# Optimization experiments

Measured on AMD Instinct MI355X. Metric: run time of the kernel, lower is better.

## Reference

```python
import jax, jax.numpy as jnp
import numpy as np
import math

IN_DIM = 128
NUM_BEV = 128
HEIGHT, WIDTH, DEPTH = 200, 176, 2  # pos_table dims: grid_size[1]//8, grid_size[0]//8, 2
PLANES = IN_DIM  # SA_block planes


def make_pos_table():
    d_model = IN_DIM
    pe = np.zeros((d_model, HEIGHT, WIDTH, DEPTH), dtype=np.float32)
    dm = int(math.ceil(d_model / 3))
    if dm % 2:
        dm += 1
    div_term = np.exp(np.arange(0.0, dm, 2) * -(math.log(10000.0) / dm))
    div_term_depth = np.exp(np.arange(0.0, dm - 2, 2) * -(math.log(10000.0) / dm - 2))
    pos_w = np.arange(0.0, WIDTH)[:, None]
    pos_h = np.arange(0.0, HEIGHT)[:, None]
    pos_d = np.arange(0.0, DEPTH)[:, None]
    sw = np.sin(pos_w * div_term).T  # [dm/2, W]
    cw = np.cos(pos_w * div_term).T
    sh = np.sin(pos_h * div_term).T  # [dm/2, H]
    ch = np.cos(pos_h * div_term).T
    sd = np.sin(pos_d * div_term_depth).T  # [.., D]
    cd = np.cos(pos_d * div_term_depth).T
    pe[0:dm:2] = np.broadcast_to(sw[:, None, :, None], (sw.shape[0], HEIGHT, WIDTH, DEPTH))
    pe[1:dm:2] = np.broadcast_to(cw[:, None, :, None], (cw.shape[0], HEIGHT, WIDTH, DEPTH))
    pe[dm:2 * dm:2] = np.broadcast_to(sh[:, :, None, None], (sh.shape[0], HEIGHT, WIDTH, DEPTH))
    pe[dm + 1:2 * dm:2] = np.broadcast_to(ch[:, :, None, None], (ch.shape[0], HEIGHT, WIDTH, DEPTH))
    n_rem_s = pe[2 * dm::2].shape[0]
    n_rem_c = pe[2 * dm + 1::2].shape[0]
    pe[2 * dm::2] = np.broadcast_to(sd[:n_rem_s, None, None, :], (n_rem_s, HEIGHT, WIDTH, DEPTH))
    pe[2 * dm + 1::2] = np.broadcast_to(cd[:n_rem_c, None, None, :], (n_rem_c, HEIGHT, WIDTH, DEPTH))
    return jnp.asarray(pe)


def sa_block(x, params):
    # x: [C, N] single-batch non-local self-attention (SA-Det3D SA_block)
    # q,k: C -> C/2 via 1x1 "conv" (matmul), grouped softmax attention, v: C -> C/2, out: C/2 -> C, residual
    r = PLANES // 2
    q = params['wq'] @ x   # [r, N]
    k = params['wk'] @ x   # [r, N]
    v = params['wv'] @ x   # [r, N]
    # scaled dot-product attention over N (groups=1 simplification of kernel_channel attention)
    q = q / jnp.sqrt(jnp.asarray(r, x.dtype))
    att = jax.nn.softmax(q.T @ k, axis=-1)  # [N, N]
    out = v @ att.T                           # [r, N]
    out = params['wo'] @ out                  # [C, N]
    # BN in eval with default init ~ identity (gamma=1, beta=0, running stats 0/1)
    return out + x


def layer_norm(x, gamma, beta, eps=1e-6):
    mu = jnp.mean(x, axis=-1, keepdims=True)
    var = jnp.var(x, axis=-1, keepdims=True)
    return (x - mu) * jax.lax.rsqrt(var + eps) * gamma + beta


def setup_inputs() -> dict:
    key = jax.random.key(0)
    ks = jax.random.split(key, 12)
    N, B = 32768, 4
    nper = N // B
    voxel_feats = jax.random.normal(ks[0], (N, IN_DIM), dtype=jnp.float32)
    b = jnp.repeat(jnp.arange(B, dtype=jnp.int32), nper)
    cz = jax.random.randint(ks[1], (N,), 0, 2, dtype=jnp.int32)
    cy = jax.random.randint(ks[2], (N,), 0, HEIGHT, dtype=jnp.int32)
    cx = jax.random.randint(ks[3], (N,), 0, WIDTH, dtype=jnp.int32)
    coords = jnp.stack([b, cz, cy, cx], axis=1)
    r = PLANES // 2
    sd = 1.0 / np.sqrt(IN_DIM)
    def mk(k, shape, s):
        return jax.random.normal(k, shape, dtype=jnp.float32) * s
    p1 = {'wq': mk(ks[4], (r, IN_DIM), sd), 'wk': mk(ks[5], (r, IN_DIM), sd),
          'wv': mk(ks[6], (r, IN_DIM), sd), 'wo': mk(ks[7], (IN_DIM, r), 1.0 / np.sqrt(r))}
    p2 = {'wq': mk(ks[8], (r, IN_DIM), sd), 'wk': mk(ks[9], (r, IN_DIM), sd),
          'wv': mk(ks[10], (r, IN_DIM), sd), 'wo': mk(ks[11], (IN_DIM, r), 1.0 / np.sqrt(r))}
    return {
        'voxel_feats': voxel_feats,
        'coords': coords,
        'ln_gamma': jnp.ones((IN_DIM,), jnp.float32),
        'ln_beta': jnp.zeros((IN_DIM,), jnp.float32),
        'attn1_wq': p1['wq'], 'attn1_wk': p1['wk'], 'attn1_wv': p1['wv'], 'attn1_wo': p1['wo'],
        'attn2_wq': p2['wq'], 'attn2_wk': p2['wk'], 'attn2_wv': p2['wv'], 'attn2_wo': p2['wo'],
        'nx': 176, 'ny': 200, 'nz': 2, 'batch_size': 4,
    }


def bilinear_down2(x):
    # F.interpolate(scale_factor=0.5, mode='bilinear', align_corners=False)
    B, C, H, W = x.shape
    return x.reshape(B, C, H // 2, 2, W // 2, 2).mean(axis=(3, 5))


def reference(voxel_feats, coords, ln_gamma, ln_beta,
              attn1_wq, attn1_wk, attn1_wv, attn1_wo,
              attn2_wq, attn2_wk, attn2_wv, attn2_wo,
              nx, ny, nz, batch_size):
    pos_table = make_pos_table()
    # positional encoding gather: pos_table[:, y, x, z] -> [C, N] -> [N, C]
    pe = pos_table[:, coords[:, 2], coords[:, 3], coords[:, 1]].T
    x = voxel_feats + jax.lax.stop_gradient(pe)
    x = layer_norm(x, ln_gamma, ln_beta)  # dropout in eval = identity

    N = x.shape[0]
    nper = N // batch_size  # fixed voxels per batch (setup guarantees contiguous equal split)
    p1 = {'wq': attn1_wq, 'wk': attn1_wk, 'wv': attn1_wv, 'wo': attn1_wo}
    p2 = {'wq': attn2_wq, 'wk': attn2_wk, 'wv': attn2_wv, 'wo': attn2_wo}

    xb = x.reshape(batch_size, nper, IN_DIM).transpose(0, 2, 1)  # [B, C, n]
    def per_batch(xc):
        return sa_block(sa_block(xc, p1), p2)
    yb = jax.vmap(per_batch)(xb)  # [B, C, n]

    cb = coords.reshape(batch_size, nper, 4)
    indices = (cb[:, :, 1] + cb[:, :, 2] * nx + cb[:, :, 3]).astype(jnp.int32)  # [B, n]
    grid = nz * nx * ny
    spatial = jnp.zeros((batch_size, NUM_BEV, grid), dtype=x.dtype)
    spatial = spatial.at[jnp.arange(batch_size)[:, None], :, indices].set(
        yb.transpose(0, 2, 1))
    out = spatial.reshape(batch_size, NUM_BEV * nz, ny, nx)
    out_half = bilinear_down2(out)
    return out, out_half
```

## Files before the change

kernel.cpp:

```cpp
#include <hip/hip_runtime.h>
#include <cmath>
#include <algorithm>

typedef __bf16 bf16x8 __attribute__((ext_vector_type(8)));
typedef float  f32x4  __attribute__((ext_vector_type(4)));
typedef unsigned int u32x2 __attribute__((ext_vector_type(2)));

struct TabArgs { double dt[22]; double dtd[21]; };

__device__ __forceinline__ unsigned short f2bf(float f) {
  unsigned int u = __float_as_uint(f);
  u += 0x7FFFu + ((u >> 16) & 1u);
  return (unsigned short)(u >> 16);
}

union U8 { uint4 u4; u32x2 d2[2]; unsigned short s[8]; bf16x8 b; };

__device__ __forceinline__ bf16x8 pack8(float4 a, float4 b) {
  U8 u;
  u.s[0] = f2bf(a.x); u.s[1] = f2bf(a.y); u.s[2] = f2bf(a.z); u.s[3] = f2bf(a.w);
  u.s[4] = f2bf(b.x); u.s[5] = f2bf(b.y); u.s[6] = f2bf(b.z); u.s[7] = f2bf(b.w);
  return u.b;
}

__device__ __forceinline__ f32x4 mfma16(bf16x8 a, bf16x8 b, f32x4 c) {
  return __builtin_amdgcn_mfma_f32_16x16x32_bf16(a, b, c, 0, 0, 0);
}

__device__ __forceinline__ unsigned ldso(const void* p) {
  return (unsigned)(unsigned long long)(const __attribute__((address_space(3))) void*)p;
}
__device__ __forceinline__ void gll16(const void* g, void* l) {
  __builtin_amdgcn_global_load_lds(
      (const __attribute__((address_space(1))) unsigned int*)g,
      (__attribute__((address_space(3))) unsigned int*)l, 16, 0, 0);
}
__device__ __forceinline__ u32x2 trd(unsigned addr) {
  u32x2 d;
  asm volatile("ds_read_b64_tr_b16 %0, %1" : "=v"(d) : "v"(addr) : "memory");
  return d;
}
__device__ __forceinline__ unsigned cvtpk(float lo, float hi) {
  unsigned r;
  asm("v_cvt_pk_bf16_f32 %0, %1, %2" : "=v"(r) : "v"(lo), "v"(hi));
  return r;
}

#define WSTRIDE 35264

__global__ __launch_bounds__(256) void k_tab(float* __restrict__ tab, TabArgs ta) {
  int t = blockIdx.x * 256 + threadIdx.x;
  if (t >= 16624) return;
  double arg; int odd;
  if (t < 7744) {
    int pos = t / 44, c = t - pos * 44; odd = c & 1;
    arg = (double)pos * ta.dt[c >> 1];
  } else if (t < 16544) {
    int u = t - 7744; int pos = u / 44, c = u - pos * 44; odd = c & 1;
    arg = (double)pos * ta.dt[c >> 1];
  } else {
    int u = t - 16544; int z = u / 40, c = u - z * 40; odd = c & 1;
    arg = z ? ta.dtd[c >> 1] : 0.0;
  }
  tab[t] = (float)(odd ? cos(arg) : sin(arg));
}

__global__ __launch_bounds__(256) void k_peln(const float* __restrict__ vox, const int* __restrict__ coords,
                                              const float* __restrict__ gamma, const float* __restrict__ beta,
                                              const float* __restrict__ tab, float* __restrict__ xo) {
  int wave = threadIdx.x >> 6, lane = threadIdx.x & 63;
  int n = blockIdx.x * 4 + wave;
  int cz = coords[n * 4 + 1], cy = coords[n * 4 + 2], cx = coords[n * 4 + 3];
  int c0 = lane, c1 = lane + 64;
  float p0 = (c0 < 44) ? tab[cx * 44 + c0] : tab[7744 + cy * 44 + (c0 - 44)];
  float p1 = (c1 < 88) ? tab[7744 + cy * 44 + (c1 - 44)] : tab[16544 + cz * 40 + (c1 - 88)];
  float x0 = vox[n * 128 + c0] + p0;
  float x1 = vox[n * 128 + c1] + p1;
  float s = x0 + x1, q = x0 * x0 + x1 * x1;
  #pragma unroll
  for (int o = 1; o < 64; o <<= 1) { s += __shfl_xor(s, o); q += __shfl_xor(q, o); }
  float mu  = s * 0.0078125f;
  float var = q * 0.0078125f - mu * mu;
  float inv = 1.0f / sqrtf(var + 1e-6f);
  xo[n * 128 + c0] = (x0 - mu) * inv * gamma[c0] + beta[c0];
  xo[n * 128 + c1] = (x1 - mu) * inv * gamma[c1] + beta[c1];
}

__global__ __launch_bounds__(192) void k_qkv(const float* __restrict__ X,
    const float* __restrict__ wq, const float* __restrict__ wk, const float* __restrict__ wv,
    unsigned short* __restrict__ Qo, unsigned short* __restrict__ Ko, unsigned short* __restrict__ Vo) {
  __shared__ uint4 xs4[1024];
  char* xs = (char*)xs4;
  int base = blockIdx.x * 64;
  for (int t = threadIdx.x; t < 1024; t += 192) {
    int row = t >> 4, ch = t & 15;
    const float* src = X + (base + row) * 128 + ch * 8;
    U8 u; u.b = pack8(*(const float4*)src, *(const float4*)(src + 4));
    *(uint4*)(xs + ((row * 256 + ch * 16) ^ ((row & 7) << 4))) = u.u4;
  }
  __syncthreads();
  int w = threadIdx.x >> 6, ln = threadIdx.x & 63, g = ln >> 4, l15 = ln & 15;
  const float* W = (w == 0) ? wq : (w == 1) ? wk : wv;
  unsigned short* O = (w == 0) ? Qo : (w == 1) ? Ko : Vo;
  f32x4 z = {0.f, 0.f, 0.f, 0.f};
  f32x4 acc[4][4];
  #pragma unroll
  for (int i = 0; i < 4; i++)
    #pragma unroll
    for (int j = 0; j < 4; j++) acc[i][j] = z;
  for (int ks = 0; ks < 4; ks++) {
    bf16x8 bf[4];
    #pragma unroll
    for (int nb = 0; nb < 4; nb++) {
      const float* wp = W + (nb * 16 + l15) * 128 + ks * 32 + g * 8;
      bf[nb] = pack8(*(const float4*)wp, *(const float4*)(wp + 4));
    }
    #pragma unroll
    for (int mb = 0; mb < 4; mb++) {
      bf16x8 af = *(const bf16x8*)(xs + (((mb * 16 + l15) * 256 + ks * 64 + g * 16) ^ ((l15 & 7) << 4)));
      #pragma unroll
      for (int nb = 0; nb < 4; nb++) acc[mb][nb] = mfma16(af, bf[nb], acc[mb][nb]);
    }
  }
  float sc = (w == 0) ? 0.125f : 1.0f;
  #pragma unroll
  for (int mb = 0; mb < 4; mb++)
    #pragma unroll
    for (int nb = 0; nb < 4; nb++)
      #pragma unroll
      for (int r = 0; r < 4; r++)
        O[(base + mb * 16 + g * 4 + r) * 64 + nb * 16 + l15] = f2bf(acc[mb][nb][r] * sc);
}

__global__ __launch_bounds__(256) void k_flash(const unsigned short* __restrict__ Qp,
    const unsigned short* __restrict__ Kp, const unsigned short* __restrict__ Vp,
    const float* __restrict__ wo, const float* __restrict__ Xin, float* __restrict__ Xout) {
  __shared__ __align__(16) char lds[40960];
  const int bid0 = blockIdx.x;
  const int bid = ((bid0 & 7) << 6) | (bid0 >> 3);
  const int qt = bid & 127, b = bid >> 7;
  const int tid = threadIdx.x;
  const int w = tid >> 6, g = (tid >> 4) & 3, l15 = tid & 15;
  const int wrow = b * 8192 + qt * 64 + w * 16;
  const int swz = (l15 & 7) << 4;
  const unsigned lb = ldso(lds);
  char* PbC = lds + 32768 + w * 2048;
  const unsigned PbA = lb + 32768u + (unsigned)w * 2048u;

  bf16x8 qf0 = *(const bf16x8*)(Qp + (wrow + l15) * 64 + g * 8);
  bf16x8 qf1 = *(const bf16x8*)(Qp + (wrow + l15) * 64 + 32 + g * 8);

  f32x4 zz = {0.f, 0.f, 0.f, 0.f};
  f32x4 o[4]; float mr[4], lr[4];
  #pragma unroll
  for (int i = 0; i < 4; i++) { o[i] = zz; mr[i] = -INFINITY; lr[i] = 0.f; }

  const int kvb0 = b * 8192;

#define STAGE(T) do {                                                          \
    int kvb_ = kvb0 + (T) * 64;                                                \
    unsigned db_ = (unsigned)((T) & 1) * 16384u;                               \
    _Pragma("unroll")                                                          \
    for (int t0 = 0; t0 < 2; t0++) {                                           \
      int u_ = tid + t0 * 256;                                                 \
      int row_ = u_ >> 3, c_ = u_ & 7;                                         \
      gll16(Kp + (kvb_ + row_) * 64 + ((c_ ^ (row_ & 7)) * 8),                 \
            lds + db_ + (unsigned)(w * 64 + t0 * 256) * 16u);                  \
      int row2_ = ((u_ >> 5) << 2) | ((u_ >> 1) & 3);                          \
      int ch2_ = (((u_ >> 3) & 3) << 1) | (u_ & 1);                            \
      gll16(Vp + (kvb_ + row2_) * 64 + ch2_ * 8,                               \
            lds + db_ + 8192u + (unsigned)(w * 64 + t0 * 256) * 16u);          \
    }                                                                          \
  } while (0)

  STAGE(0);
  __syncthreads();

  for (int kt = 0; kt < 128; kt++) {
    const unsigned kbB = (unsigned)(kt & 1) * 16384u;
    const unsigned vbB = kbB + 8192u;
    if (kt < 127) STAGE(kt + 1);

    f32x4 s[4];
    #pragma unroll
    for (int kb = 0; kb < 4; kb++) {
      bf16x8 kf0 = *(const bf16x8*)(lds + kbB + (unsigned)((((kb * 16 + l15) * 128 + g * 16) ^ swz)));
      bf16x8 kf1 = *(const bf16x8*)(lds + kbB + (unsigned)((((kb * 16 + l15) * 128 + 64 + g * 16) ^ swz)));
      s[kb] = mfma16(qf0, kf0, zz);
      s[kb] = mfma16(qf1, kf1, s[kb]);
    }
    float al[4];
    #pragma unroll
    for (int r = 0; r < 4; r++) {
      float mx = fmaxf(fmaxf(s[0][r], s[1][r]), fmaxf(s[2][r], s[3][r]));
      #pragma unroll
      for (int off = 1; off < 16; off <<= 1) mx = fmaxf(mx, __shfl_xor(mx, off));
      float mn = fmaxf(mr[r], mx);
      al[r] = __expf(mr[r] - mn);
      float p0 = __expf(s[0][r] - mn), p1 = __expf(s[1][r] - mn);
      float p2 = __expf(s[2][r] - mn), p3 = __expf(s[3][r] - mn);
      s[0][r] = p0; s[1][r] = p1; s[2][r] = p2; s[3][r] = p3;
      lr[r] = lr[r] * al[r] + ((p0 + p1) + (p2 + p3));
      mr[r] = mn;
    }
    #pragma unroll
    for (int db = 0; db < 4; db++)
      #pragma unroll
      for (int r = 0; r < 4; r++) o[db][r] *= al[r];

    #pragma unroll
    for (int kb = 0; kb < 4; kb++) {
      u32x2 pw;
      pw.x = cvtpk(s[kb][0], s[kb][1]);
      pw.y = cvtpk(s[kb][2], s[kb][3]);
      *(u32x2*)(PbC + (kb * 4 + (l15 >> 2)) * 128 + (l15 & 3) * 32 + g * 8) = pw;
    }
    asm volatile("s_waitcnt lgkmcnt(0)" ::: "memory");
    __builtin_amdgcn_sched_barrier(0);

    #pragma unroll
    for (int kc = 0; kc < 2; kc++) {
      unsigned preg = PbA + (unsigned)((kc * 8 + g * 2) * 128 + l15 * 8);
      u32x2 pa0 = trd(preg);
      u32x2 pa1 = trd(preg + 128u);
      unsigned vreg = lb + vbB + (unsigned)((kc * 8 + g * 2) * 512 + l15 * 8);
      u32x2 v00 = trd(vreg);          u32x2 v01 = trd(vreg + 512u);
      u32x2 v10 = trd(vreg + 128u);   u32x2 v11 = trd(vreg + 640u);
      u32x2 v20 = trd(vreg + 256u);   u32x2 v21 = trd(vreg + 768u);
      u32x2 v30 = trd(vreg + 384u);   u32x2 v31 = trd(vreg + 896u);
      asm volatile("s_waitcnt lgkmcnt(0)" ::: "memory");
      __builtin_amdgcn_sched_barrier(0);
      U8 ua;  ua.d2[0] = pa0;  ua.d2[1] = pa1;
      U8 u0;  u0.d2[0] = v00;  u0.d2[1] = v01;
      U8 u1;  u1.d2[0] = v10;  u1.d2[1] = v11;
      U8 u2;  u2.d2[0] = v20;  u2.d2[1] = v21;
      U8 u3;  u3.d2[0] = v30;  u3.d2[1] = v31;
      o[0] = mfma16(ua.b, u0.b, o[0]);
      o[1] = mfma16(ua.b, u1.b, o[1]);
      o[2] = mfma16(ua.b, u2.b, o[2]);
      o[3] = mfma16(ua.b, u3.b, o[3]);
    }
    __syncthreads();
  }

  #pragma unroll
  for (int r = 0; r < 4; r++)
    #pragma unroll
    for (int off = 1; off < 16; off <<= 1) lr[r] += __shfl_xor(lr[r], off);
  float iv[4];
  #pragma unroll
  for (int r = 0; r < 4; r++) iv[r] = 1.0f / lr[r];
  #pragma unroll
  for (int db = 0; db < 4; db++)
    #pragma unroll
    for (int r = 0; r < 4; r++) {
      int q = g * 4 + r;
      *(unsigned short*)(PbC + ((q * 128 + (db * 16 + l15) * 2) ^ ((q & 7) << 4))) = f2bf(o[db][r] * iv[r]);
    }
  __syncthreads();
  f32x4 a2[8];
  #pragma unroll
  for (int cb = 0; cb < 8; cb++) a2[cb] = zz;
  #pragma unroll
  for (int ksx = 0; ksx < 2; ksx++) {
    bf16x8 oa = *(const bf16x8*)(PbC + ((l15 * 128 + ksx * 64 + g * 16) ^ swz));
    #pragma unroll
    for (int cb = 0; cb < 8; cb++) {
      const float* wp = wo + (cb * 16 + l15) * 64 + ksx * 32 + g * 8;
      a2[cb] = mfma16(oa, pack8(*(const float4*)wp, *(const float4*)(wp + 4)), a2[cb]);
    }
  }
  #pragma unroll
  for (int cb = 0; cb < 8; cb++)
    #pragma unroll
    for (int r = 0; r < 4; r++) {
      int row = wrow + g * 4 + r, col = cb * 16 + l15;
      Xout[row * 128 + col] = a2[cb][r] + Xin[row * 128 + col];
    }
#undef STAGE
}

__global__ __launch_bounds__(256) void k_win(const int* __restrict__ coords, int* __restrict__ win) {
  int n = blockIdx.x * 256 + threadIdx.x;
  int b = n >> 13, j = n & 8191;
  int cz = coords[n * 4 + 1], cy = coords[n * 4 + 2], cx = coords[n * 4 + 3];
  int idx = cz + cy * 176 + cx;
  atomicMax(&win[b * WSTRIDE + idx], j);
}

__global__ __launch_bounds__(256) void k_gp(const int* __restrict__ win, const float* __restrict__ X,
                                            float* __restrict__ out, float* __restrict__ half_) {
  unsigned tid = blockIdx.x * 256u + threadIdx.x;
  unsigned b = tid / 2252800u;
  unsigned f = tid % 2252800u;
  unsigned ch2 = f / 8800u;
  unsigned rem = f % 8800u;
  unsigned yh = rem / 88u, xh = rem % 88u;
  unsigned c = ch2 >> 1;
  unsigned zoff = (ch2 & 1u) * 35200u;
  const int* wb = win + b * WSTRIDE;
  const float* Xb = X + (unsigned long long)b * 8192u * 128u + c;
  unsigned y0 = 2u * yh, x0 = 2u * xh;
  float v[4];
  #pragma unroll
  for (int dy = 0; dy < 2; dy++)
    #pragma unroll
    for (int dx = 0; dx < 2; dx++) {
      unsigned gcell = zoff + (y0 + dy) * 176u + (x0 + dx);
      float val = 0.f;
      if (gcell <= 35200u) {
        int j = wb[gcell];
        if (j >= 0) val = Xb[(unsigned)j * 128u];
      }
      v[dy * 2 + dx] = val;
    }
  float* ob = out + (((unsigned long long)(b * 256u + ch2)) * 200u + y0) * 176u + x0;
  ob[0] = v[0]; ob[1] = v[1]; ob[176] = v[2]; ob[177] = v[3];
  half_[tid] = 0.25f * ((v[0] + v[1]) + (v[2] + v[3]));
}

namespace ddm {
struct dd { double h, l; };
static inline dd qts(double a, double b) { double s = a + b; return {s, b - (s - a)}; }
static inline dd tsum(double a, double b) {
  double s = a + b, bb = s - a; return {s, (a - (s - bb)) + (b - bb)};
}
static inline dd tprod(double a, double b) { double p = a * b; return {p, std::fma(a, b, -p)}; }
static inline dd dadd(dd a, dd b) { dd s = tsum(a.h, b.h); double l = s.l + a.l + b.l; return qts(s.h, l); }
static inline dd dmul(dd a, dd b) {
  dd p = tprod(a.h, b.h); double l = p.l + (a.h * b.l + a.l * b.h); return qts(p.h, l);
}
static inline dd dmuld(dd a, double b) { dd p = tprod(a.h, b); double l = p.l + a.l * b; return qts(p.h, l); }
static inline dd dinv(double n) { double h = 1.0 / n; double l = std::fma(-h, n, 1.0) / n; return {h, l}; }
static inline dd dsqrt(dd a) {
  double s = std::sqrt(a.h);
  dd s2 = tprod(s, s);
  dd e = dadd(a, {-s2.h, -s2.l});
  double c = (e.h + e.l) / (2.0 * s);
  return qts(s, c);
}
struct ExpCtx {
  dd ln2_64;
  dd tab[64];
  ExpCtx() {
    dd third = dinv(3.0);
    dd t2 = dmul(third, third);
    dd pw = third, s = {0.0, 0.0};
    for (int k = 0; k < 42; k++) {
      s = dadd(s, dmul(pw, dinv((double)(2 * k + 1))));
      pw = dmul(pw, t2);
    }
    dd ln2 = {2.0 * s.h, 2.0 * s.l};
    ln2_64 = {ln2.h / 64.0, ln2.l / 64.0};
    dd r = {2.0, 0.0};
    for (int i = 0; i < 6; i++) r = dsqrt(r);
    tab[0] = {1.0, 0.0};
    for (int j = 1; j < 64; j++) tab[j] = dmul(tab[j - 1], r);
  }
  double exp(double x) const {
    if (x == 0.0) return 1.0;
    double m = std::nearbyint(x * (64.0 / 0.6931471805599453));
    dd r = dadd({x, 0.0}, dmuld(ln2_64, -m));
    dd s = {1.0, 0.0}, term = {1.0, 0.0};
    for (int k = 1; k <= 13; k++) {
      term = dmul(term, r);
      term = dmul(term, dinv((double)k));
      s = dadd(s, term);
    }
    long mi = (long)m;
    long e = mi >> 6;
    long j = mi & 63;
    dd v = dmul(tab[j], s);
    return std::scalbn(v.h + v.l, (int)e);
  }
};
}

extern "C" void kernel_launch(void* const* d_in, const int* in_sizes, int n_in,
                              void* d_out, int out_size, void* d_ws, size_t ws_size,
                              hipStream_t stream) {
  const float* vox   = (const float*)d_in[0];
  const int*   coords= (const int*)d_in[1];
  const float* gam   = (const float*)d_in[2];
  const float* bet   = (const float*)d_in[3];
  const float* w1q = (const float*)d_in[4], *w1k = (const float*)d_in[5];
  const float* w1v = (const float*)d_in[6], *w1o = (const float*)d_in[7];
  const float* w2q = (const float*)d_in[8], *w2k = (const float*)d_in[9];
  const float* w2v = (const float*)d_in[10], *w2o = (const float*)d_in[11];
  float* out = (float*)d_out;
  char* ws = (char*)d_ws;

  float* tab  = (float*)(ws);
  int*   win  = (int*)(ws + 69632);
  float* bufA = (float*)(ws + 1048576);
  float* bufB = (float*)(ws + 18874368);
  unsigned short* Q = (unsigned short*)(ws + 37748736);
  unsigned short* K = (unsigned short*)(ws + 41943040);
  unsigned short* V = (unsigned short*)(ws + 46137344);

  ddm::ExpCtx ec;
  TabArgs ta;
  double lg = std::log(10000.0);
  double t1 = -(lg / 44.0);
  double t2 = -(lg / 44.0 - 2.0);
  for (int i = 0; i < 22; i++) ta.dt[i]  = ec.exp((double)(2 * i) * t1);
  for (int i = 0; i < 21; i++) ta.dtd[i] = ec.exp((double)(2 * i) * t2);

  {
    const double E0 = 0.245;
    const int RANK = 0;
    struct Cand { double score; int i; int d; };
    Cand cands[20]; int nc = 0;
    for (int i = 10; i <= 19; i++) {
      double c = ta.dtd[i];
      double u = std::nextafter(c, 1e300) - c;
      for (int d = -1; d <= 1; d += 2) {
        double cp = c + (double)d * u;
        double es = std::fabs(std::sin(cp) - std::sin(c));
        double ecs = std::fabs(std::cos(cp) - std::cos(c));
        double e = es > ecs ? es : ecs;
        cands[nc++] = { std::fabs(e - E0), i, d };
      }
    }
    std::sort(cands, cands + nc, [](const Cand& a, const Cand& b){ return a.score < b.score; });
    if (RANK < nc) {
      double c = ta.dtd[cands[RANK].i];
      double u = std::nextafter(c, 1e300) - c;
      ta.dtd[cands[RANK].i] = c + (double)cands[RANK].d * u;
    }
  }

  hipMemsetAsync(win, 0xFF, 4 * WSTRIDE * sizeof(int), stream);
  hipLaunchKernelGGL(k_tab,   dim3(65),     dim3(256), 0, stream, tab, ta);
  hipLaunchKernelGGL(k_peln,  dim3(8192),   dim3(256), 0, stream, vox, coords, gam, bet, tab, bufA);
  hipLaunchKernelGGL(k_qkv,   dim3(512),    dim3(192), 0, stream, bufA, w1q, w1k, w1v, Q, K, V);
  hipLaunchKernelGGL(k_flash, dim3(512),    dim3(256), 0, stream, Q, K, V, w1o, bufA, bufB);
  hipLaunchKernelGGL(k_qkv,   dim3(512),    dim3(192), 0, stream, bufB, w2q, w2k, w2v, Q, K, V);
  hipLaunchKernelGGL(k_flash, dim3(512),    dim3(256), 0, stream, Q, K, V, w2o, bufB, bufA);
  hipLaunchKernelGGL(k_win,   dim3(128),    dim3(256), 0, stream, coords, win);
  hipLaunchKernelGGL(k_gp,    dim3(35200),  dim3(256), 0, stream, win, bufA, out, out + 36044800);
}
```

Measured before the change: 677.6 us.

## Widen flash KV tiles to 128, defer rescaling, use exp2 and DPP reductions

The flash-attention loop now stages 128 keys per iteration instead of 64, halving the number of iterations and barriers, with LDS doubled to 80KB. The Q scale folds in log2(e) so softmax can use the raw v_exp_f32 instruction. Row max and sum reductions use DPP row_ror instead of shuffles. The running max and output rescale are skipped unless some row's max grows by more than 8. P·V transposed LDS reads are double-buffered with partial waitcnts, and setprio is placed around the MFMA sections. The larger LDS footprint may lower occupancy, and the lazy rescale lets intermediate values grow larger, which may affect precision.

Result: faster. 562.1 us (-17.0%).

```diff
diff --git a/kernel.cpp b/kernel.cpp
--- a/kernel.cpp
+++ b/kernel.cpp
@@ -45,6 +45,17 @@
   asm("v_cvt_pk_bf16_f32 %0, %1, %2" : "=v"(r) : "v"(lo), "v"(hi));
   return r;
 }
+__device__ __forceinline__ float exp2a(float x) {
+  float r;
+  asm("v_exp_f32 %0, %1" : "=v"(r) : "v"(x));
+  return r;
+}
+#define RORMAX(x, N) ({ float r_; \
+  asm("v_max_f32 %0, %1, %1 row_ror:" #N " row_mask:0xf bank_mask:0xf" \
+      : "=v"(r_) : "v"(x)); r_; })
+#define RORADD(x, N) ({ float r_; \
+  asm("v_add_f32 %0, %1, %1 row_ror:" #N " row_mask:0xf bank_mask:0xf" \
+      : "=v"(r_) : "v"(x)); r_; })
 
 #define WSTRIDE 35264
 
@@ -122,7 +133,7 @@
       for (int nb = 0; nb < 4; nb++) acc[mb][nb] = mfma16(af, bf[nb], acc[mb][nb]);
     }
   }
-  float sc = (w == 0) ? 0.125f : 1.0f;
+  float sc = (w == 0) ? 0.180336880111120428f : 1.0f;
   #pragma unroll
   for (int mb = 0; mb < 4; mb++)
     #pragma unroll
@@ -135,7 +146,7 @@
 __global__ __launch_bounds__(256) void k_flash(const unsigned short* __restrict__ Qp,
     const unsigned short* __restrict__ Kp, const unsigned short* __restrict__ Vp,
     const float* __restrict__ wo, const float* __restrict__ Xin, float* __restrict__ Xout) {
-  __shared__ __align__(16) char lds[40960];
+  __shared__ __align__(16) char lds[81920];
   const int bid0 = blockIdx.x;
   const int bid = ((bid0 & 7) << 6) | (bid0 >> 3);
   const int qt = bid & 127, b = bid >> 7;
@@ -144,8 +155,8 @@
   const int wrow = b * 8192 + qt * 64 + w * 16;
   const int swz = (l15 & 7) << 4;
   const unsigned lb = ldso(lds);
-  char* PbC = lds + 32768 + w * 2048;
-  const unsigned PbA = lb + 32768u + (unsigned)w * 2048u;
+  char* PbC = lds + 65536 + w * 4096;
+  const unsigned PbA = lb + 65536u + (unsigned)w * 4096u;
 
   bf16x8 qf0 = *(const bf16x8*)(Qp + (wrow + l15) * 64 + g * 8);
   bf16x8 qf1 = *(const bf16x8*)(Qp + (wrow + l15) * 64 + 32 + g * 8);
@@ -158,10 +169,10 @@
   const int kvb0 = b * 8192;
 
 #define STAGE(T) do {                                                          \
-    int kvb_ = kvb0 + (T) * 64;                                                \
-    unsigned db_ = (unsigned)((T) & 1) * 16384u;                               \
+    int kvb_ = kvb0 + (T) * 128;                                               \
+    unsigned db_ = (unsigned)((T) & 1) * 32768u;                               \
     _Pragma("unroll")                                                          \
-    for (int t0 = 0; t0 < 2; t0++) {                                           \
+    for (int t0 = 0; t0 < 4; t0++) {                                           \
       int u_ = tid + t0 * 256;                                                 \
       int row_ = u_ >> 3, c_ = u_ & 7;                                         \
       gll16(Kp + (kvb_ + row_) * 64 + ((c_ ^ (row_ & 7)) * 8),                 \
@@ -169,47 +180,69 @@
       int row2_ = ((u_ >> 5) << 2) | ((u_ >> 1) & 3);                          \
       int ch2_ = (((u_ >> 3) & 3) << 1) | (u_ & 1);                            \
       gll16(Vp + (kvb_ + row2_) * 64 + ch2_ * 8,                               \
-            lds + db_ + 8192u + (unsigned)(w * 64 + t0 * 256) * 16u);          \
+            lds + db_ + 16384u + (unsigned)(w * 64 + t0 * 256) * 16u);         \
     }                                                                          \
   } while (0)
 
   STAGE(0);
   __syncthreads();
 
-  for (int kt = 0; kt < 128; kt++) {
-    const unsigned kbB = (unsigned)(kt & 1) * 16384u;
-    const unsigned vbB = kbB + 8192u;
-    if (kt < 127) STAGE(kt + 1);
-
-    f32x4 s[4];
-    #pragma unroll
-    for (int kb = 0; kb < 4; kb++) {
+  for (int kt = 0; kt < 64; kt++) {
+    const unsigned kbB = (unsigned)(kt & 1) * 32768u;
+    const unsigned vbB = kbB + 16384u;
+    if (kt < 63) STAGE(kt + 1);
+
+    f32x4 s[8];
+    __builtin_amdgcn_s_setprio(1);
+    #pragma unroll
+    for (int kb = 0; kb < 8; kb++) {
       bf16x8 kf0 = *(const bf16x8*)(lds + kbB + (unsigned)((((kb * 16 + l15) * 128 + g * 16) ^ swz)));
       bf16x8 kf1 = *(const bf16x8*)(lds + kbB + (unsigned)((((kb * 16 + l15) * 128 + 64 + g * 16) ^ swz)));
       s[kb] = mfma16(qf0, kf0, zz);
       s[kb] = mfma16(qf1, kf1, s[kb]);
     }
-    float al[4];
+    __builtin_amdgcn_s_setprio(0);
+
+    float mx[4];
     #pragma unroll
     for (int r = 0; r < 4; r++) {
-      float mx = fmaxf(fmaxf(s[0][r], s[1][r]), fmaxf(s[2][r], s[3][r]));
+      float m0 = fmaxf(fmaxf(s[0][r], s[1][r]), fmaxf(s[2][r], s[3][r]));
+      float m1 = fmaxf(fmaxf(s[4][r], s[5][r]), fmaxf(s[6][r], s[7][r]));
+      float m = fmaxf(m0, m1);
+      m = RORMAX(m, 1); m = RORMAX(m, 2); m = RORMAX(m, 4); m = RORMAX(m, 8);
+      mx[r] = m;
+    }
+    float g01 = fmaxf(mx[0] - mr[0], mx[1] - mr[1]);
+    float g23 = fmaxf(mx[2] - mr[2], mx[3] - mr[3]);
+    if (!__all(fmaxf(g01, g23) <= 8.0f)) {
+      float al[4];
       #pragma unroll
-      for (int off = 1; off < 16; off <<= 1) mx = fmaxf(mx, __shfl_xor(mx, off));
-      float mn = fmaxf(mr[r], mx);
-      al[r] = __expf(mr[r] - mn);
-      float p0 = __expf(s[0][r] - mn), p1 = __expf(s[1][r] - mn);
-      float p2 = __expf(s[2][r] - mn), p3 = __expf(s[3][r] - mn);
-      s[0][r] = p0; s[1][r] = p1; s[2][r] = p2; s[3][r] = p3;
-      lr[r] = lr[r] * al[r] + ((p0 + p1) + (p2 + p3));
-      mr[r] = mn;
-    }
-    #pragma unroll
-    for (int db = 0; db < 4; db++)
+      for (int r = 0; r < 4; r++) {
+        float mn = fmaxf(mr[r], mx[r]);
+        float a = exp2a(mr[r] - mn);
+        lr[r] *= a;
+        mr[r] = mn;
+        al[r] = a;
+      }
       #pragma unroll
-      for (int r = 0; r < 4; r++) o[db][r] *= al[r];
-
-    #pragma unroll
-    for (int kb = 0; kb < 4; kb++) {
+      for (int db = 0; db < 4; db++)
+        #pragma unroll
+        for (int r = 0; r < 4; r++) o[db][r] *= al[r];
+    }
+    #pragma unroll
+    for (int r = 0; r < 4; r++) {
+      float ps = 0.f;
+      #pragma unroll
+      for (int kb = 0; kb < 8; kb++) {
+        float p = exp2a(s[kb][r] - mr[r]);
+        s[kb][r] = p;
+        ps += p;
+      }
+      lr[r] += ps;
+    }
+
+    #pragma unroll
+    for (int kb = 0; kb < 8; kb++) {
       u32x2 pw;
       pw.x = cvtpk(s[kb][0], s[kb][1]);
       pw.y = cvtpk(s[kb][2], s[kb][3]);
@@ -218,35 +251,49 @@
     asm volatile("s_waitcnt lgkmcnt(0)" ::: "memory");
     __builtin_amdgcn_sched_barrier(0);
 
-    #pragma unroll
-    for (int kc = 0; kc < 2; kc++) {
-      unsigned preg = PbA + (unsigned)((kc * 8 + g * 2) * 128 + l15 * 8);
-      u32x2 pa0 = trd(preg);
-      u32x2 pa1 = trd(preg + 128u);
-      unsigned vreg = lb + vbB + (unsigned)((kc * 8 + g * 2) * 512 + l15 * 8);
-      u32x2 v00 = trd(vreg);          u32x2 v01 = trd(vreg + 512u);
-      u32x2 v10 = trd(vreg + 128u);   u32x2 v11 = trd(vreg + 640u);
-      u32x2 v20 = trd(vreg + 256u);   u32x2 v21 = trd(vreg + 768u);
-      u32x2 v30 = trd(vreg + 384u);   u32x2 v31 = trd(vreg + 896u);
-      asm volatile("s_waitcnt lgkmcnt(0)" ::: "memory");
+    struct Batch { u32x2 pa0, pa1, vv[8]; };
+    Batch bt[2];
+#define ISSUE(KC, SL) do {                                                       \
+      unsigned preg_ = PbA + (unsigned)((((KC) * 8 + g * 2) * 128 + l15 * 8));   \
+      bt[SL].pa0 = trd(preg_);            bt[SL].pa1 = trd(preg_ + 128u);        \
+      unsigned vreg_ = lb + vbB + (unsigned)((((KC) * 8 + g * 2) * 512 + l15 * 8)); \
+      bt[SL].vv[0] = trd(vreg_);          bt[SL].vv[1] = trd(vreg_ + 512u);      \
+      bt[SL].vv[2] = trd(vreg_ + 128u);   bt[SL].vv[3] = trd(vreg_ + 640u);      \
+      bt[SL].vv[4] = trd(vreg_ + 256u);   bt[SL].vv[5] = trd(vreg_ + 768u);      \
+      bt[SL].vv[6] = trd(vreg_ + 384u);   bt[SL].vv[7] = trd(vreg_ + 896u);      \
+    } while (0)
+    ISSUE(0, 0);
+    #pragma unroll
+    for (int kc = 0; kc < 4; kc++) {
+      const int cur = kc & 1;
+      if (kc == 0) { ISSUE(1, 1); }
+      else if (kc == 1) { ISSUE(2, 0); }
+      else if (kc == 2) { ISSUE(3, 1); }
+      if (kc < 3) { asm volatile("s_waitcnt lgkmcnt(10)" ::: "memory"); }
+      else        { asm volatile("s_waitcnt lgkmcnt(0)"  ::: "memory"); }
       __builtin_amdgcn_sched_barrier(0);
-      U8 ua;  ua.d2[0] = pa0;  ua.d2[1] = pa1;
-      U8 u0;  u0.d2[0] = v00;  u0.d2[1] = v01;
-      U8 u1;  u1.d2[0] = v10;  u1.d2[1] = v11;
-      U8 u2;  u2.d2[0] = v20;  u2.d2[1] = v21;
-      U8 u3;  u3.d2[0] = v30;  u3.d2[1] = v31;
+      U8 ua; ua.d2[0] = bt[cur].pa0;   ua.d2[1] = bt[cur].pa1;
+      U8 u0; u0.d2[0] = bt[cur].vv[0]; u0.d2[1] = bt[cur].vv[1];
+      U8 u1; u1.d2[0] = bt[cur].vv[2]; u1.d2[1] = bt[cur].vv[3];
+      U8 u2; u2.d2[0] = bt[cur].vv[4]; u2.d2[1] = bt[cur].vv[5];
+      U8 u3; u3.d2[0] = bt[cur].vv[6]; u3.d2[1] = bt[cur].vv[7];
+      __builtin_amdgcn_s_setprio(1);
       o[0] = mfma16(ua.b, u0.b, o[0]);
       o[1] = mfma16(ua.b, u1.b, o[1]);
       o[2] = mfma16(ua.b, u2.b, o[2]);
       o[3] = mfma16(ua.b, u3.b, o[3]);
-    }
+      __builtin_amdgcn_s_setprio(0);
+    }
+#undef ISSUE
     __syncthreads();
   }
 
   #pragma unroll
-  for (int r = 0; r < 4; r++)
-    #pragma unroll
-    for (int off = 1; off < 16; off <<= 1) lr[r] += __shfl_xor(lr[r], off);
+  for (int r = 0; r < 4; r++) {
+    float t = lr[r];
+    t = RORADD(t, 1); t = RORADD(t, 2); t = RORADD(t, 4); t = RORADD(t, 8);
+    lr[r] = t;
+  }
   float iv[4];
   #pragma unroll
   for (int r = 0; r < 4; r++) iv[r] = 1.0f / lr[r];
```
